# Optimization experiments

Hardware: AMD Instinct MI355X
Metric: run time of the kernel (lower is better)

## Reference

```python
import jax, jax.numpy as jnp
import numpy as np


def _bitlinear(x, W, b):
    # BitNet 1.58 absmean ternary quantization with STE.
    gamma = jnp.abs(W).mean() + 1e-8
    w_tern = jnp.clip(jnp.round(W / gamma), -1.0, 1.0)
    # STE: forward uses ternary weights, gradient flows to W.
    w_ste = w_tern + (W - jax.lax.stop_gradient(W))
    return x @ w_ste.T + b


def _gelu(x):
    return jax.nn.gelu(x, approximate=False)  # torch nn.GELU default is exact erf


def setup_inputs() -> dict:
    key = jax.random.key(0)
    ks = jax.random.split(key, 16)
    B, H = 8192, 2048
    dims = [2048, 1024, 512, 256]  # encoder: 2048->1024->512->256
    inp = {
        "z": jax.random.normal(ks[0], (B, H // 2), jnp.float32),
        "attention_out": jax.random.normal(ks[1], (B, H // 2), jnp.float32),
    }
    ki = 2
    for l in range(3):
        inp[f"We{l}"] = jax.random.normal(ks[ki], (dims[l + 1], dims[l]), jnp.float32) * 0.02
        inp[f"be{l}"] = jnp.zeros((dims[l + 1],), jnp.float32)
        ki += 1
    inp["Wb"] = jax.random.normal(ks[ki], (256, 256), jnp.float32) * 0.02
    inp["bb"] = jnp.zeros((256,), jnp.float32)
    ki += 1
    for l in range(3):  # decoder: 256->512->1024->2048
        inp[f"Wd{l}"] = jax.random.normal(ks[ki], (dims[2 - l], dims[3 - l]), jnp.float32) * 0.02
        inp[f"bd{l}"] = jnp.zeros((dims[2 - l],), jnp.float32)
        ki += 1
    return inp


def reference(z, attention_out, We0, be0, We1, be1, We2, be2, Wb, bb,
              Wd0, bd0, Wd1, bd1, Wd2, bd2):
    x = jnp.concatenate([z, attention_out], axis=-1)  # (B, 2048)
    skips = []
    for W, b in [(We0, be0), (We1, be1), (We2, be2)]:
        x = _gelu(_bitlinear(x, W, b))
        skips.append(x)
    x = _gelu(_bitlinear(x, Wb, bb))
    for i, (W, b) in enumerate([(Wd0, bd0), (Wd1, bd1), (Wd2, bd2)]):
        x = _bitlinear(x, W, b)
        skip = skips[-(i + 1)]
        if x.shape[-1] == skip.shape[-1]:  # static dim check; never true for this config
            x = x + skip
        x = _gelu(x)
    return x
```

## Files before the change

kernel.cpp:

```cpp
#include <hip/hip_runtime.h>
#include <hip/hip_bf16.h>
#include <cstdint>

typedef __attribute__((ext_vector_type(8))) __bf16 bf16x8;
typedef __attribute__((ext_vector_type(4))) float f32x4;

typedef __attribute__((address_space(1))) const void g_void;
typedef __attribute__((address_space(3))) void l_void;

__device__ __forceinline__ void gload_lds16(const void* g, void* l) {
  __builtin_amdgcn_global_load_lds((g_void*)(uintptr_t)g,
                                   (l_void*)(uint32_t)(uintptr_t)l, 16, 0, 0);
}

__device__ __forceinline__ ushort f2bf(float f) {
  union { float f; uint32_t u; } v; v.f = f;
  uint32_t r = v.u + 0x7fffu + ((v.u >> 16) & 1u);
  return (ushort)(r >> 16);
}

struct WDesc {
  const float* W[7];
  int nvec[7];
  int vcum[8];
};

__global__ void absmean_partial(WDesc wd, float* __restrict__ partials) {
  __shared__ float red[256];
  const int layer = blockIdx.y;
  const float4* W = (const float4*)wd.W[layer];
  const int nv = wd.nvec[layer];
  float s = 0.f;
  for (int i = blockIdx.x * 256 + threadIdx.x; i < nv; i += gridDim.x * 256) {
    float4 w = W[i];
    s += fabsf(w.x) + fabsf(w.y) + fabsf(w.z) + fabsf(w.w);
  }
  red[threadIdx.x] = s;
  __syncthreads();
  for (int o = 128; o > 0; o >>= 1) {
    if (threadIdx.x < o) red[threadIdx.x] += red[threadIdx.x + o];
    __syncthreads();
  }
  if (threadIdx.x == 0) partials[layer * 64 + blockIdx.x] = red[0];
}

__global__ void absmean_final(WDesc wd, const float* __restrict__ partials,
                              float* __restrict__ ig) {
  const int layer = blockIdx.x;
  float v = partials[layer * 64 + threadIdx.x];
  for (int o = 32; o > 0; o >>= 1) v += __shfl_down(v, o, 64);
  if (threadIdx.x == 0) {
    float mean = v / (float)(wd.nvec[layer] * 4);
    ig[layer] = 1.0f / (mean + 1e-8f);
  }
}

__global__ void prep_kernel(WDesc wd, const float* __restrict__ ig,
                            ushort* __restrict__ qw,
                            const float* __restrict__ z,
                            const float* __restrict__ att,
                            ushort* __restrict__ cat, int qblks) {
  if ((int)blockIdx.x < qblks) {
    const int v = blockIdx.x * 256 + threadIdx.x;
    if (v >= wd.vcum[7]) return;
    int layer = 0;
#pragma unroll
    for (int i = 1; i < 7; ++i) layer += (v >= wd.vcum[i]);
    const int lv = v - wd.vcum[layer];
    const float g = ig[layer];
    float4 w = ((const float4*)wd.W[layer])[lv];
    ushort4 o;
    o.x = f2bf(fmaxf(-1.f, fminf(1.f, rintf(w.x * g))));
    o.y = f2bf(fmaxf(-1.f, fminf(1.f, rintf(w.y * g))));
    o.z = f2bf(fmaxf(-1.f, fminf(1.f, rintf(w.z * g))));
    o.w = f2bf(fmaxf(-1.f, fminf(1.f, rintf(w.w * g))));
    ((ushort4*)qw)[v] = o;
  } else {
    const int tg = (blockIdx.x - qblks) * 256 + threadIdx.x;
    const int row = tg >> 8;
    const int k0 = (tg & 255) * 8;
    const float* src = (k0 < 1024) ? (z + (size_t)row * 1024 + k0)
                                   : (att + (size_t)row * 1024 + (k0 - 1024));
    float4 a = ((const float4*)src)[0];
    float4 b = ((const float4*)src)[1];
    ushort4 o0; o0.x = f2bf(a.x); o0.y = f2bf(a.y); o0.z = f2bf(a.z); o0.w = f2bf(a.w);
    ushort4 o1; o1.x = f2bf(b.x); o1.y = f2bf(b.y); o1.z = f2bf(b.z); o1.w = f2bf(b.w);
    ushort4* dst = (ushort4*)(cat + (size_t)tg * 8);
    dst[0] = o0; dst[1] = o1;
  }
}

__device__ __forceinline__ float gelu_fast(float x) {
  float x2 = x * x;
  float u = x * fmaf(x2, 0.0356774081f, 0.7978845608f);
  float e = exp2f(u * 2.8853900818f);
  float r = __builtin_amdgcn_rcpf(e + 1.0f);
  return x - x * r;
}

#define SB0() __builtin_amdgcn_sched_barrier(0)
#define BAR() __builtin_amdgcn_s_barrier()
#define LGKM0() asm volatile("s_waitcnt lgkmcnt(0)" ::: "memory")
#define VMW(NN) asm volatile("s_waitcnt vmcnt(%0)" ::"n"(NN) : "memory")

template <int BN, bool OUT_F32>
__global__ __launch_bounds__(512, 2)
void gemm_pipe3(const ushort* __restrict__ A, const ushort* __restrict__ Bw,
                const float* __restrict__ bias, void* __restrict__ Cv,
                int M, int N, int K) {
  constexpr int BM = 256;
  constexpr int WN = BN / 4;
  constexpr int FM = 8;
  constexpr int FN = WN / 16;
  constexpr int HM = 4;
  constexpr int HN = 1;
  constexpr int SA = 4;
  constexpr int SB = BN / 64;
  constexpr int L = SA + SB;
  constexpr int TILE_USH = (BM + BN) * 64;

  __shared__ ushort lds[3 * TILE_USH];

  const int t = threadIdx.x;
  const int lane = t & 63, wid = t >> 6;
  const int wr = wid >> 2, wc = wid & 3;
  const int l15 = lane & 15, lhi = lane >> 4;

  const int gx = gridDim.x;
  const int nwg = gx * gridDim.y;
  int lin = blockIdx.y * gx + blockIdx.x;
  lin = (lin & 7) * (nwg >> 3) + (lin >> 3);
  const int bm0 = (lin / gx) * BM, bn0 = (lin % gx) * BN;

  const int NT = K >> 6;

  const int srow = t >> 3;
  const int scol = ((t & 7) ^ ((t >> 3) & 7)) * 8;

  auto stage = [&](int tile, int buf) {
    ushort* tb = &lds[buf * TILE_USH];
    const int kt = tile * 64;
#pragma unroll
    for (int c = 0; c < SA; ++c) {
      const int lr = c * 64 + srow;
      gload_lds16(A + (size_t)(bm0 + lr) * K + kt + scol,
                  &tb[lr * 64 + (t & 7) * 8]);
    }
#pragma unroll
    for (int c = 0; c < SB; ++c) {
      const int lr = c * 64 + srow;
      gload_lds16(Bw + (size_t)(bn0 + lr) * K + kt + scol,
                  &tb[BM * 64 + lr * 64 + (t & 7) * 8]);
    }
  };

  bf16x8 a[HM][2], b[HN][2];
  f32x4 acc[FM][FN] = {};

  auto loadA = [&](const ushort* tb, int mh) {
#pragma unroll
    for (int mi = 0; mi < HM; ++mi) {
      const int row = wr * 128 + (mh * HM + mi) * 16 + l15;
#pragma unroll
      for (int kh = 0; kh < 2; ++kh)
        a[mi][kh] =
            *(const bf16x8*)&tb[row * 64 + ((kh * 4 + lhi) ^ (l15 & 7)) * 8];
    }
  };
  auto loadB = [&](const ushort* tb, int nh) {
#pragma unroll
    for (int ni = 0; ni < HN; ++ni) {
      const int row = wc * WN + (nh * HN + ni) * 16 + l15;
#pragma unroll
      for (int kh = 0; kh < 2; ++kh)
        b[ni][kh] = *(const bf16x8*)&tb[BM * 64 + row * 64 +
                                        ((kh * 4 + lhi) ^ (l15 & 7)) * 8];
    }
  };

#define MFMA_(MH, NH)                                                        \
  {                                                                          \
    __builtin_amdgcn_s_setprio(1);                                           \
    _Pragma("unroll") for (int kh = 0; kh < 2; ++kh)                         \
    _Pragma("unroll") for (int mi = 0; mi < HM; ++mi)                        \
    _Pragma("unroll") for (int ni = 0; ni < HN; ++ni)                        \
      acc[(MH) * HM + mi][(NH) * HN + ni] =                                  \
          __builtin_amdgcn_mfma_f32_16x16x32_bf16(                           \
              a[mi][kh], b[ni][kh], acc[(MH) * HM + mi][(NH) * HN + ni],     \
              0, 0, 0);                                                      \
    __builtin_amdgcn_s_setprio(0);                                           \
  }

  stage(0, 0);
  stage(1, 1);
  VMW(L);
  BAR();
  SB0();

  int buf = 0, sbuf = 2;
  for (int tt = 0; tt < NT; ++tt) {
    const bool more = (tt + 2 < NT);
    if (more) stage(tt + 2, sbuf);
    const ushort* tb = &lds[buf * TILE_USH];
    if constexpr (FN == 2) {
      loadA(tb, 0); loadB(tb, 0);
      MFMA_(0, 0);
      loadB(tb, 1);
      MFMA_(0, 1);
      loadA(tb, 1);
      MFMA_(1, 1);
      loadB(tb, 0);
      MFMA_(1, 0);
    } else {
      loadA(tb, 0); loadB(tb, 0);
      MFMA_(0, 0);
      loadA(tb, 1);
      MFMA_(1, 0);
    }
    SB0();
    if (more) { VMW(L); } else { VMW(0); }
    BAR();
    SB0();
    buf = (buf == 2) ? 0 : buf + 1;
    sbuf = (sbuf == 2) ? 0 : sbuf + 1;
  }
#undef MFMA_

#pragma unroll
  for (int n = 0; n < FN; ++n) {
    const int col = bn0 + wc * WN + n * 16 + l15;
    const float bv = bias[col];
#pragma unroll
    for (int m = 0; m < FM; ++m) {
      const int row0 = bm0 + wr * 128 + m * 16 + lhi * 4;
#pragma unroll
      for (int j = 0; j < 4; ++j) {
        float v = acc[m][n][j] + bv;
        float gv = gelu_fast(v);
        if (OUT_F32)
          ((float*)Cv)[(size_t)(row0 + j) * N + col] = gv;
        else
          ((ushort*)Cv)[(size_t)(row0 + j) * N + col] = f2bf(gv);
      }
    }
  }
}

template <bool OUT_F32>
__global__ __launch_bounds__(512, 1)
void gemm_8ph(const ushort* __restrict__ A, const ushort* __restrict__ Bw,
              const float* __restrict__ bias, void* __restrict__ Cv,
              int M, int N, int K) {
  constexpr int BM = 256;
  constexpr int BN = 256;
  constexpr int WN = 64;
  constexpr int FM = 8;
  constexpr int FN = 4;
  constexpr int HM = 4;
  constexpr int HN = 2;
  constexpr int TILE_USH = (BM + BN) * 64;

  __shared__ ushort lds[2 * TILE_USH];

  const int t = threadIdx.x;
  const int lane = t & 63, wid = t >> 6;
  const int wr = wid >> 2, wc = wid & 3;
  const int l15 = lane & 15, lhi = lane >> 4;

  const int gx = gridDim.x;
  const int nwg = gx * gridDim.y;
  int lin = blockIdx.y * gx + blockIdx.x;
  lin = (lin & 7) * (nwg >> 3) + (lin >> 3);
  const int bm0 = (lin / gx) * BM, bn0 = (lin % gx) * BN;

  const int NT = K >> 6;

  const int srow = t >> 3;
  const int scol = ((t & 7) ^ ((t >> 3) & 7)) * 8;

  auto stageA2 = [&](ushort* tb, int kt, int h) {
#pragma unroll
    for (int c = 0; c < 2; ++c) {
      const int lr = h * 128 + c * 64 + srow;
      gload_lds16(A + (size_t)(bm0 + lr) * K + kt + scol,
                  &tb[lr * 64 + (t & 7) * 8]);
    }
  };
  auto stageB2 = [&](ushort* tb, int kt, int h) {
#pragma unroll
    for (int c = 0; c < 2; ++c) {
      const int lr = h * 128 + c * 64 + srow;
      gload_lds16(Bw + (size_t)(bn0 + lr) * K + kt + scol,
                  &tb[BM * 64 + lr * 64 + (t & 7) * 8]);
    }
  };

  bf16x8 a[HM][2], b[HN][2];
  f32x4 acc[FM][FN] = {};

  auto loadA = [&](const ushort* tb, int mh) {
#pragma unroll
    for (int mi = 0; mi < HM; ++mi) {
      const int row = wr * 128 + (mh * HM + mi) * 16 + l15;
#pragma unroll
      for (int kh = 0; kh < 2; ++kh)
        a[mi][kh] =
            *(const bf16x8*)&tb[row * 64 + ((kh * 4 + lhi) ^ (l15 & 7)) * 8];
    }
  };
  auto loadB = [&](const ushort* tb, int nh) {
#pragma unroll
    for (int ni = 0; ni < HN; ++ni) {
      const int row = wc * WN + (nh * HN + ni) * 16 + l15;
#pragma unroll
      for (int kh = 0; kh < 2; ++kh)
        b[ni][kh] = *(const bf16x8*)&tb[BM * 64 + row * 64 +
                                        ((kh * 4 + lhi) ^ (l15 & 7)) * 8];
    }
  };

#define MFMA_(MH, NH)                                                        \
  {                                                                          \
    __builtin_amdgcn_s_setprio(1);                                           \
    _Pragma("unroll") for (int kh = 0; kh < 2; ++kh)                         \
    _Pragma("unroll") for (int mi = 0; mi < HM; ++mi)                        \
    _Pragma("unroll") for (int ni = 0; ni < HN; ++ni)                        \
      acc[(MH) * HM + mi][(NH) * HN + ni] =                                  \
          __builtin_amdgcn_mfma_f32_16x16x32_bf16(                           \
              a[mi][kh], b[ni][kh], acc[(MH) * HM + mi][(NH) * HN + ni],     \
              0, 0, 0);                                                      \
    __builtin_amdgcn_s_setprio(0);                                           \
  }

  stageB2(&lds[0], 0, 0);
  stageB2(&lds[0], 0, 1);
  stageA2(&lds[0], 0, 0);
  stageA2(&lds[0], 0, 1);
  VMW(2);
  BAR();
  SB0();

  for (int J = 0; J < NT; ++J) {
    const ushort* tb = &lds[(J & 1) * TILE_USH];
    ushort* sb = &lds[((J & 1) ^ 1) * TILE_USH];
    const int kt2 = (J + 1) << 6;
    const bool more = (J + 1) < NT;

    loadA(tb, 0);
    loadB(tb, 0);
    if (more) stageB2(sb, kt2, 0);
    BAR();
    LGKM0();
    SB0();
    MFMA_(0, 0);
    SB0();
    BAR();
    SB0();

    loadB(tb, 1);
    if (more) stageB2(sb, kt2, 1);
    BAR();
    LGKM0();
    SB0();
    MFMA_(0, 1);
    SB0();
    if (more) { VMW(4); } else { VMW(0); }
    BAR();
    SB0();

    loadA(tb, 1);
    if (more) stageA2(sb, kt2, 0);
    BAR();
    LGKM0();
    SB0();
    MFMA_(1, 1);
    SB0();
    BAR();
    SB0();

    loadB(tb, 0);
    if (more) stageA2(sb, kt2, 1);
    BAR();
    LGKM0();
    SB0();
    MFMA_(1, 0);
    SB0();
    if (more) { VMW(2); } else { VMW(0); }
    BAR();
    SB0();
  }
#undef MFMA_

#pragma unroll
  for (int n = 0; n < FN; ++n) {
    const int col = bn0 + wc * WN + n * 16 + l15;
    const float bv = bias[col];
#pragma unroll
    for (int m = 0; m < FM; ++m) {
      const int row0 = bm0 + wr * 128 + m * 16 + lhi * 4;
#pragma unroll
      for (int j = 0; j < 4; ++j) {
        float v = acc[m][n][j] + bv;
        float gv = gelu_fast(v);
        if (OUT_F32)
          ((float*)Cv)[(size_t)(row0 + j) * N + col] = gv;
        else
          ((ushort*)Cv)[(size_t)(row0 + j) * N + col] = f2bf(gv);
      }
    }
  }
}

template <int BM, int BN, bool OUT_F32>
__global__ __launch_bounds__(256, 4)
void gemm_bt_bias_gelu(const ushort* __restrict__ A, const ushort* __restrict__ Bw,
                       const float* __restrict__ bias, void* __restrict__ Cv,
                       int M, int N, int K) {
  constexpr int WTM = BM / 32;
  constexpr int WTN = BN / 32;
  __shared__ ushort As[BM * 64];
  __shared__ ushort Bs[BN * 64];
  const int t = threadIdx.x;
  const int lane = t & 63, wid = t >> 6;
  const int wr = wid >> 1, wc = wid & 1;
  const int l15 = lane & 15, lhi = lane >> 4;

  const int gx = gridDim.x;
  const int nwg = gx * gridDim.y;
  int lin = blockIdx.y * gx + blockIdx.x;
  if ((nwg & 7) == 0) lin = (lin & 7) * (nwg >> 3) + (lin >> 3);
  const int bm0 = (lin / gx) * BM, bn0 = (lin % gx) * BN;

  const ushort* Abase = A + (size_t)bm0 * K;
  const ushort* Bbase = Bw + (size_t)bn0 * K;

  f32x4 acc[WTM][WTN] = {};

  for (int kt = 0; kt < K; kt += 64) {
#pragma unroll
    for (int i = 0; i < BM / 32; ++i) {
      int c = i * 256 + t;
      int r = c >> 3, c8 = c & 7;
      gload_lds16(Abase + (size_t)r * K + kt + c8 * 8, &As[c * 8]);
    }
#pragma unroll
    for (int i = 0; i < BN / 32; ++i) {
      int c = i * 256 + t;
      int r = c >> 3, c8 = c & 7;
      gload_lds16(Bbase + (size_t)r * K + kt + c8 * 8, &Bs[c * 8]);
    }
    asm volatile("s_waitcnt vmcnt(0)" ::: "memory");
    __syncthreads();
#pragma unroll
    for (int kk = 0; kk < 64; kk += 32) {
      bf16x8 af[WTM], bfr[WTN];
#pragma unroll
      for (int m = 0; m < WTM; ++m)
        af[m] = *(const bf16x8*)&As[(wr * (BM / 2) + m * 16 + l15) * 64 + kk + lhi * 8];
#pragma unroll
      for (int n = 0; n < WTN; ++n)
        bfr[n] = *(const bf16x8*)&Bs[(wc * (BN / 2) + n * 16 + l15) * 64 + kk + lhi * 8];
#pragma unroll
      for (int m = 0; m < WTM; ++m)
#pragma unroll
        for (int n = 0; n < WTN; ++n)
          acc[m][n] = __builtin_amdgcn_mfma_f32_16x16x32_bf16(af[m], bfr[n], acc[m][n], 0, 0, 0);
    }
    __syncthreads();
  }

#pragma unroll
  for (int n = 0; n < WTN; ++n) {
    const int col = bn0 + wc * (BN / 2) + n * 16 + l15;
    const float bv = bias[col];
#pragma unroll
    for (int m = 0; m < WTM; ++m) {
      const int row0 = bm0 + wr * (BM / 2) + m * 16 + lhi * 4;
#pragma unroll
      for (int j = 0; j < 4; ++j) {
        float v = acc[m][n][j] + bv;
        float gv = gelu_fast(v);
        if (OUT_F32)
          ((float*)Cv)[(size_t)(row0 + j) * N + col] = gv;
        else
          ((ushort*)Cv)[(size_t)(row0 + j) * N + col] = f2bf(gv);
      }
    }
  }
}

extern "C" void kernel_launch(void* const* d_in, const int* in_sizes, int n_in,
                              void* d_out, int out_size, void* d_ws, size_t ws_size,
                              hipStream_t stream) {
  const float* z   = (const float*)d_in[0];
  const float* att = (const float*)d_in[1];
  const float* Wptr[7] = {(const float*)d_in[2],  (const float*)d_in[4],
                          (const float*)d_in[6],  (const float*)d_in[8],
                          (const float*)d_in[10], (const float*)d_in[12],
                          (const float*)d_in[14]};
  const float* bptr[7] = {(const float*)d_in[3],  (const float*)d_in[5],
                          (const float*)d_in[7],  (const float*)d_in[9],
                          (const float*)d_in[11], (const float*)d_in[13],
                          (const float*)d_in[15]};
  const int Ns[7] = {1024, 512, 256, 256, 512, 1024, 2048};
  const int Ks[7] = {2048, 1024, 512, 256, 256, 512, 1024};
  const int M = 8192;

  char* ws = (char*)d_ws;
  ushort* bufA = (ushort*)ws;
  ushort* bufB = (ushort*)(ws + 33554432);
  ushort* qw   = (ushort*)(ws + 33554432 + 16777216);
  float* partials = (float*)(ws + 33554432 + 16777216 + 11141120);
  float* ig = partials + 7 * 64;

  WDesc wd;
  int cum = 0;
  size_t qoff[7]; size_t qc = 0;
  for (int l = 0; l < 7; ++l) {
    wd.W[l] = Wptr[l];
    int nv = Ns[l] * Ks[l] / 4;
    wd.nvec[l] = nv;
    wd.vcum[l] = cum;
    cum += nv;
    qoff[l] = qc;
    qc += (size_t)Ns[l] * Ks[l];
  }
  wd.vcum[7] = cum;

  const int qblks = (cum + 255) / 256;
  absmean_partial<<<dim3(64, 7), 256, 0, stream>>>(wd, partials);
  absmean_final<<<7, 64, 0, stream>>>(wd, partials, ig);
  prep_kernel<<<qblks + 8192, 256, 0, stream>>>(wd, ig, qw, z, att, bufA, qblks);

  ushort* inb = bufA; ushort* outb = bufB;
  gemm_pipe3<128, false><<<dim3(Ns[0] / 128, M / 256), dim3(512), 0, stream>>>(
      inb, qw + qoff[0], bptr[0], outb, M, Ns[0], Ks[0]);
  { ushort* tmp = inb; inb = outb; outb = tmp; }
  gemm_pipe3<64, false><<<dim3(Ns[1] / 64, M / 256), dim3(512), 0, stream>>>(
      inb, qw + qoff[1], bptr[1], outb, M, Ns[1], Ks[1]);
  { ushort* tmp = inb; inb = outb; outb = tmp; }
  gemm_bt_bias_gelu<64, 64, false><<<dim3(Ns[2] / 64, M / 64), 256, 0, stream>>>(
      inb, qw + qoff[2], bptr[2], outb, M, Ns[2], Ks[2]);
  { ushort* tmp = inb; inb = outb; outb = tmp; }
  gemm_bt_bias_gelu<64, 64, false><<<dim3(Ns[3] / 64, M / 64), 256, 0, stream>>>(
      inb, qw + qoff[3], bptr[3], outb, M, Ns[3], Ks[3]);
  { ushort* tmp = inb; inb = outb; outb = tmp; }
  gemm_pipe3<64, false><<<dim3(Ns[4] / 64, M / 256), dim3(512), 0, stream>>>(
      inb, qw + qoff[4], bptr[4], outb, M, Ns[4], Ks[4]);
  { ushort* tmp = inb; inb = outb; outb = tmp; }
  gemm_pipe3<128, false><<<dim3(Ns[5] / 128, M / 256), dim3(512), 0, stream>>>(
      inb, qw + qoff[5], bptr[5], outb, M, Ns[5], Ks[5]);
  { ushort* tmp = inb; inb = outb; outb = tmp; }
  gemm_8ph<true><<<dim3(Ns[6] / 256, M / 256), dim3(512), 0, stream>>>(
      inb, qw + qoff[6], bptr[6], d_out, M, Ns[6], Ks[6]);
}
```

Baseline: 186.2 us.

## Restructure final GEMM pipeline to prefetch A two tiles ahead with register double-buffering

The final 256x256-tile GEMM kernel now holds both halves of the A and B fragments in registers instead of one half. That removes the redundant B reload in the last phase. The A tile for iteration J+2 is staged into the current LDS buffer once its fragments are in registers, while B for J+1 goes into the other buffer, which deepens the global-to-LDS prefetch. The launch bound is raised to request two workgroups per CU. The 128 KB LDS footprint cannot fit two workgroups, and the tighter register budget this bound implies, next to the 128-register accumulator, risks spills. The wait-count bookkeeping also changes, which adds correctness risk.

```diff
diff --git a/kernel.cpp b/kernel.cpp
--- a/kernel.cpp
+++ b/kernel.cpp
@@ -247,17 +247,12 @@
 }
 
 template <bool OUT_F32>
-__global__ __launch_bounds__(512, 1)
-void gemm_8ph(const ushort* __restrict__ A, const ushort* __restrict__ Bw,
+__global__ __launch_bounds__(512, 2)
+void gemm_8p2(const ushort* __restrict__ A, const ushort* __restrict__ Bw,
               const float* __restrict__ bias, void* __restrict__ Cv,
               int M, int N, int K) {
   constexpr int BM = 256;
   constexpr int BN = 256;
-  constexpr int WN = 64;
-  constexpr int FM = 8;
-  constexpr int FN = 4;
-  constexpr int HM = 4;
-  constexpr int HN = 2;
   constexpr int TILE_USH = (BM + BN) * 64;
 
   __shared__ ushort lds[2 * TILE_USH];
@@ -278,44 +273,45 @@
   const int srow = t >> 3;
   const int scol = ((t & 7) ^ ((t >> 3) & 7)) * 8;
 
-  auto stageA2 = [&](ushort* tb, int kt, int h) {
+  auto stageA = [&](ushort* tb, int kt, int h) {
 #pragma unroll
     for (int c = 0; c < 2; ++c) {
       const int lr = h * 128 + c * 64 + srow;
-      gload_lds16(A + (size_t)(bm0 + lr) * K + kt + scol,
+      gload_lds16(A + (size_t)(bm0 + lr) * K + kt * 64 + scol,
                   &tb[lr * 64 + (t & 7) * 8]);
     }
   };
-  auto stageB2 = [&](ushort* tb, int kt, int h) {
+  auto stageB = [&](ushort* tb, int kt, int h) {
 #pragma unroll
     for (int c = 0; c < 2; ++c) {
       const int lr = h * 128 + c * 64 + srow;
-      gload_lds16(Bw + (size_t)(bn0 + lr) * K + kt + scol,
+      gload_lds16(Bw + (size_t)(bn0 + lr) * K + kt * 64 + scol,
                   &tb[BM * 64 + lr * 64 + (t & 7) * 8]);
     }
   };
 
-  bf16x8 a[HM][2], b[HN][2];
-  f32x4 acc[FM][FN] = {};
+  bf16x8 a[2][4][2];
+  bf16x8 b[2][2][2];
+  f32x4 acc[8][4] = {};
 
   auto loadA = [&](const ushort* tb, int mh) {
 #pragma unroll
-    for (int mi = 0; mi < HM; ++mi) {
-      const int row = wr * 128 + (mh * HM + mi) * 16 + l15;
+    for (int mi = 0; mi < 4; ++mi) {
+      const int row = wr * 128 + mh * 64 + mi * 16 + l15;
 #pragma unroll
       for (int kh = 0; kh < 2; ++kh)
-        a[mi][kh] =
+        a[mh][mi][kh] =
             *(const bf16x8*)&tb[row * 64 + ((kh * 4 + lhi) ^ (l15 & 7)) * 8];
     }
   };
   auto loadB = [&](const ushort* tb, int nh) {
 #pragma unroll
-    for (int ni = 0; ni < HN; ++ni) {
-      const int row = wc * WN + (nh * HN + ni) * 16 + l15;
+    for (int ni = 0; ni < 2; ++ni) {
+      const int row = wc * 64 + nh * 32 + ni * 16 + l15;
 #pragma unroll
       for (int kh = 0; kh < 2; ++kh)
-        b[ni][kh] = *(const bf16x8*)&tb[BM * 64 + row * 64 +
-                                        ((kh * 4 + lhi) ^ (l15 & 7)) * 8];
+        b[nh][ni][kh] = *(const bf16x8*)&tb[BM * 64 + row * 64 +
+                                            ((kh * 4 + lhi) ^ (l15 & 7)) * 8];
     }
   };
 
@@ -323,32 +319,36 @@
   {                                                                          \
     __builtin_amdgcn_s_setprio(1);                                           \
     _Pragma("unroll") for (int kh = 0; kh < 2; ++kh)                         \
-    _Pragma("unroll") for (int mi = 0; mi < HM; ++mi)                        \
-    _Pragma("unroll") for (int ni = 0; ni < HN; ++ni)                        \
-      acc[(MH) * HM + mi][(NH) * HN + ni] =                                  \
+    _Pragma("unroll") for (int mi = 0; mi < 4; ++mi)                         \
+    _Pragma("unroll") for (int ni = 0; ni < 2; ++ni)                         \
+      acc[(MH) * 4 + mi][(NH) * 2 + ni] =                                    \
           __builtin_amdgcn_mfma_f32_16x16x32_bf16(                           \
-              a[mi][kh], b[ni][kh], acc[(MH) * HM + mi][(NH) * HN + ni],     \
-              0, 0, 0);                                                      \
+              a[(MH)][mi][kh], b[(NH)][ni][kh],                              \
+              acc[(MH) * 4 + mi][(NH) * 2 + ni], 0, 0, 0);                   \
     __builtin_amdgcn_s_setprio(0);                                           \
   }
 
-  stageB2(&lds[0], 0, 0);
-  stageB2(&lds[0], 0, 1);
-  stageA2(&lds[0], 0, 0);
-  stageA2(&lds[0], 0, 1);
-  VMW(2);
-  BAR();
-  SB0();
+  {
+    ushort* b0 = &lds[0];
+    ushort* b1 = &lds[TILE_USH];
+    stageA(b0, 0, 0); stageA(b0, 0, 1);
+    stageB(b0, 0, 0); stageB(b0, 0, 1);
+    stageA(b1, 1, 0); stageA(b1, 1, 1);
+    VMW(4);
+    BAR();
+    SB0();
+  }
 
   for (int J = 0; J < NT; ++J) {
     const ushort* tb = &lds[(J & 1) * TILE_USH];
-    ushort* sb = &lds[((J & 1) ^ 1) * TILE_USH];
-    const int kt2 = (J + 1) << 6;
-    const bool more = (J + 1) < NT;
+    ushort* cb = &lds[(J & 1) * TILE_USH];
+    ushort* sb = &lds[((J + 1) & 1) * TILE_USH];
+    const bool s1 = (J + 1) < NT;
+    const bool s2 = (J + 2) < NT;
 
     loadA(tb, 0);
     loadB(tb, 0);
-    if (more) stageB2(sb, kt2, 0);
+    if (s1) stageB(sb, J + 1, 0);
     BAR();
     LGKM0();
     SB0();
@@ -357,46 +357,42 @@
     BAR();
     SB0();
 
+    loadA(tb, 1);
     loadB(tb, 1);
-    if (more) stageB2(sb, kt2, 1);
+    if (s1) stageB(sb, J + 1, 1);
     BAR();
     LGKM0();
     SB0();
+    MFMA_(1, 1);
+    SB0();
+    BAR();
+    SB0();
+
+    if (s2) stageA(cb, J + 2, 0);
+    BAR();
+    SB0();
     MFMA_(0, 1);
     SB0();
-    if (more) { VMW(4); } else { VMW(0); }
-    BAR();
-    SB0();
-
-    loadA(tb, 1);
-    if (more) stageA2(sb, kt2, 0);
-    BAR();
-    LGKM0();
-    SB0();
-    MFMA_(1, 1);
-    SB0();
-    BAR();
-    SB0();
-
-    loadB(tb, 0);
-    if (more) stageA2(sb, kt2, 1);
-    BAR();
-    LGKM0();
+    BAR();
+    SB0();
+
+    if (s2) stageA(cb, J + 2, 1);
+    BAR();
     SB0();
     MFMA_(1, 0);
     SB0();
-    if (more) { VMW(2); } else { VMW(0); }
+    if (s2) { VMW(4); } else { VMW(0); }
     BAR();
     SB0();
   }
 #undef MFMA_
 
 #pragma unroll
-  for (int n = 0; n < FN; ++n) {
-    const int col = bn0 + wc * WN + n * 16 + l15;
+  for (int n = 0; n < 4; ++n) {
+    const int col = bn0 + wc * 64 + n * 16 + l15;
     const float bv = bias[col];
 #pragma unroll
-    for (int m = 0; m < FM; ++m) {
+    for (int m = 0; m < 8; ++m) {
       const int row0 = bm0 + wr * 128 + m * 16 + lhi * 4;
 #pragma unroll
       for (int j = 0; j < 4; ++j) {
@@ -551,6 +547,6 @@
   gemm_pipe3<128, false><<<dim3(Ns[5] / 128, M / 256), dim3(512), 0, stream>>>(
       inb, qw + qoff[5], bptr[5], outb, M, Ns[5], Ks[5]);
   { ushort* tmp = inb; inb = outb; outb = tmp; }
-  gemm_8ph<true><<<dim3(Ns[6] / 256, M / 256), dim3(512), 0, stream>>>(
+  gemm_8p2<true><<<dim3(Ns[6] / 256, M / 256), dim3(512), 0, stream>>>(
       inb, qw + qoff[6], bptr[6], d_out, M, Ns[6], Ks[6]);
 }
```

Result: no change. 184.6 us (-0.9%).
